# Performance work log

Hardware: AMD Instinct MI355X
Metric: run time of the kernel (lower is better)

The kernel has to match this reference:

```python
import jax, jax.numpy as jnp
import numpy as np

N, D, H, G = 4096, 256, 4, 16
HEAD_DIM = D // H
LN_EPS = 1e-5
TEMP = 5.0


def setup_inputs() -> dict:
    key = jax.random.key(0)
    ks = jax.random.split(key, 12)
    s = 0.05  # weight init scale
    nrm = lambda k, shp: jax.random.normal(k, shp, jnp.float32) * s
    return {
        "x": jax.random.normal(ks[0], (N, D), jnp.float32),
        "Wq": nrm(ks[1], (D, D)), "bq": jnp.zeros((D,), jnp.float32),
        "Wk": nrm(ks[2], (D, D)), "bk": jnp.zeros((D,), jnp.float32),
        "Wv": nrm(ks[3], (D, D)), "bv": jnp.zeros((D,), jnp.float32),
        "Wv1": nrm(ks[4], (D, D // 2)), "bv1": jnp.zeros((D // 2,), jnp.float32),
        "Wv2": nrm(ks[5], (D // 2, 1)), "bv2": jnp.zeros((1,), jnp.float32),
        "Wc1": nrm(ks[6], (2 * D, D)), "bc1": jnp.zeros((D,), jnp.float32),
        "Wc2": nrm(ks[7], (D, 1)), "bc2": jnp.zeros((1,), jnp.float32),
        "gamma": jnp.ones((D,), jnp.float32),
        "beta": jnp.zeros((D,), jnp.float32),
        "batch": jnp.sort(jax.random.randint(ks[8], (N,), 0, G)),
    }


def reference(x, Wq, bq, Wk, bk, Wv, bv, Wv1, bv1, Wv2, bv2,
              Wc1, bc1, Wc2, bc2, gamma, beta, batch):
    n = x.shape[0]
    # multi-head projections -> [N, H, head_dim]
    Q = (x @ Wq + bq).reshape(n, H, HEAD_DIM)
    K = (x @ Wk + bk).reshape(n, H, HEAD_DIM)
    V = (x @ Wv + bv).reshape(n, H, HEAD_DIM)

    # dense scores [N, N, H], block-diagonal mask by graph membership
    scores = jnp.einsum('nhd,mhd->nmh', Q, K) / np.sqrt(HEAD_DIM).astype(np.float32)
    same_graph = (batch[:, None] == batch[None, :])  # [N, N]
    scores = jnp.where(same_graph[:, :, None], scores, -jnp.inf)
    probs = jax.nn.softmax(scores, axis=1)  # softmax over keys m (dim=1, as in torch)
    # dropout is identity in eval mode
    attended = jnp.einsum('nmh,mhd->nhd', probs, V).reshape(n, D)

    # vulnerability detector MLP: D -> D/2 -> 1, sigmoid
    vuln = jax.nn.sigmoid(jax.nn.relu(x @ Wv1 + bv1) @ Wv2 + bv2)[:, 0]

    # global max pool per graph, broadcast back to nodes
    graph_ctx = jax.ops.segment_max(x, batch, num_segments=G, indices_are_sorted=True)[batch]
    combined = jnp.concatenate([x, graph_ctx], axis=1)  # [N, 2D]
    ctx = jax.nn.sigmoid(jnp.tanh(combined @ Wc1 + bc1) @ Wc2 + bc2)[:, 0]

    mha_avg = probs.mean(axis=(1, 2))  # [N]
    w = 0.6 * vuln + 0.3 * ctx + 0.1 * mha_avg

    # per-graph segment softmax with temperature 5.0
    w5 = w * TEMP
    seg_max = jax.ops.segment_max(w5, batch, num_segments=G, indices_are_sorted=True)[batch]
    e = jnp.exp(w5 - seg_max)
    seg_sum = jax.ops.segment_sum(e, batch, num_segments=G, indices_are_sorted=True)[batch]
    att = e / seg_sum  # [N]

    out = attended * att[:, None] + x  # residual
    # LayerNorm over last dim
    mu = out.mean(axis=-1, keepdims=True)
    var = out.var(axis=-1, keepdims=True)
    out = (out - mu) * jax.lax.rsqrt(var + LN_EPS) * gamma + beta
    return out, att
```

## Files before the change

kernel.cpp:

```cpp
#include <hip/hip_runtime.h>
#include <math.h>

#define N_NODES 4096
#define DIM 256
#define NH 4
#define NG 16
#define LN_EPS 1e-5f
#define TEMP 5.0f
#define RSLACK 4160
#define PS_STRIDE 72
#define BS_STRIDE 264
#define QT_MAX 24
#define K2_ATTN_BLOCKS (NG * QT_MAX)

typedef __attribute__((ext_vector_type(8))) short short8;
typedef __attribute__((ext_vector_type(4))) short short4_t;
typedef __attribute__((ext_vector_type(4))) float f32x4;

__device__ __forceinline__ unsigned short f2bf(float f) {
    unsigned u = __builtin_bit_cast(unsigned, f);
    u += 0x7FFFu + ((u >> 16) & 1u);
    return (unsigned short)(u >> 16);
}
__device__ __forceinline__ float bf2f(unsigned short u) {
    return __builtin_bit_cast(float, (unsigned)u << 16);
}
__device__ __forceinline__ float fsigmoid(float z) { return 1.f / (1.f + __expf(-z)); }
__device__ __forceinline__ float ftanh(float z) {
    float t = __expf(2.f * z);
    return (t - 1.f) / (t + 1.f);
}
__device__ __forceinline__ int seg_search(const int* __restrict__ batch, int g) {
    int lo = 0, hi = N_NODES;
    while (lo < hi) {
        int mid = (lo + hi) >> 1;
        if (batch[mid] < g) lo = mid + 1; else hi = mid;
    }
    return lo;
}

__device__ __forceinline__ short8 afrag_f32(const float* __restrict__ x, int row, int k0) {
    float4 a = *(const float4*)&x[(size_t)row * 256 + k0];
    float4 b = *(const float4*)&x[(size_t)row * 256 + k0 + 4];
    short8 r = {(short)f2bf(a.x), (short)f2bf(a.y), (short)f2bf(a.z), (short)f2bf(a.w),
                (short)f2bf(b.x), (short)f2bf(b.y), (short)f2bf(b.z), (short)f2bf(b.w)};
    return r;
}

__device__ __forceinline__ void ldsB(const float* __restrict__ W, int ws, int bn,
                                     unsigned short* __restrict__ Bs) {
    int c4 = (threadIdx.x & 15) * 4;
    int r0 = threadIdx.x >> 4;
    for (int p = 0; p < 16; ++p) {
        int k = p * 16 + r0;
        float4 wv = *(const float4*)&W[(size_t)k * ws + bn + c4];
        Bs[(c4 + 0) * BS_STRIDE + k] = f2bf(wv.x);
        Bs[(c4 + 1) * BS_STRIDE + k] = f2bf(wv.y);
        Bs[(c4 + 2) * BS_STRIDE + k] = f2bf(wv.z);
        Bs[(c4 + 3) * BS_STRIDE + k] = f2bf(wv.w);
    }
    __syncthreads();
}

__global__ __launch_bounds__(256) void k1_kernel(
    const float* __restrict__ x,
    const float* __restrict__ Wq, const float* __restrict__ bq,
    const float* __restrict__ Wk, const float* __restrict__ bk,
    const float* __restrict__ Wv, const float* __restrict__ bv,
    const float* __restrict__ Wv1, const float* __restrict__ bv1,
    const float* __restrict__ Wv2, const float* __restrict__ Wc1,
    const float* __restrict__ bc1, const int* __restrict__ batch,
    unsigned short* __restrict__ Qb, unsigned short* __restrict__ Kb,
    unsigned short* __restrict__ Vt, float* __restrict__ vacc2,
    float* __restrict__ Tpre, float* __restrict__ gcw, int* __restrict__ seg) {
    __shared__ __align__(16) char smem[64 * BS_STRIDE * 2];
    int id = blockIdx.x, tid = threadIdx.x;
    if (id < 16) {
        int g = id;
        int s = seg_search(batch, g), e = seg_search(batch, g + 1);
        float* red = (float*)smem;
        float* gl  = (float*)smem + 1024;
        int c4 = (tid & 63) * 4, way = tid >> 6;
        float4 mx = {-INFINITY, -INFINITY, -INFINITY, -INFINITY};
#pragma unroll 8
        for (int i = s + way; i < e; i += 4) {
            float4 v = *(const float4*)&x[(size_t)i * DIM + c4];
            mx.x = fmaxf(mx.x, v.x); mx.y = fmaxf(mx.y, v.y);
            mx.z = fmaxf(mx.z, v.z); mx.w = fmaxf(mx.w, v.w);
        }
        *(float4*)&red[way * 256 + c4] = mx;
        __syncthreads();
        if (way == 0) {
#pragma unroll
            for (int j = 0; j < 4; ++j) {
                float mm = fmaxf(fmaxf(red[c4 + j], red[256 + c4 + j]),
                                 fmaxf(red[512 + c4 + j], red[768 + c4 + j]));
                gl[c4 + j] = bf2f(f2bf(mm));
            }
        }
        __syncthreads();
        float ac[4] = {0.f, 0.f, 0.f, 0.f};
        for (int kb = 0; kb < 256; kb += 32) {
            float v[32];
#pragma unroll
            for (int j = 0; j < 32; ++j)
                v[j] = Wc1[(size_t)(256 + kb + j) * 256 + tid];
#pragma unroll
            for (int j = 0; j < 32; ++j) ac[j & 3] += gl[kb + j] * v[j];
        }
        gcw[g * 256 + tid] = (ac[0] + ac[1]) + (ac[2] + ac[3]);
        return;
    }
    if (id == 16) {
        if (tid <= NG) seg[tid] = seg_search(batch, tid);
        return;
    }
    int u = id - 17;
    unsigned short* Bs = (unsigned short*)smem;
    int w = tid >> 6, lane = tid & 63, m = lane & 15, quad = lane >> 4;
    if (u < 768) {
        int z = u >> 8, r = u & 255, bx = r & 63, by = r >> 6;
        const float* W = (z == 0) ? Wq : (z == 1) ? Wk : Wv;
        const float* bias = (z == 0) ? bq : (z == 1) ? bk : bv;
        ldsB(W, 256, by * 64, Bs);
        int rowA = bx * 64 + 16 * w + m;
        short8 a[8];
#pragma unroll
        for (int ks = 0; ks < 8; ++ks) a[ks] = afrag_f32(x, rowA, ks * 32 + quad * 8);
        int node0 = bx * 64 + 16 * w + quad * 4;
#pragma unroll
        for (int nt = 0; nt < 4; ++nt) {
            f32x4 acc = {0.f, 0.f, 0.f, 0.f};
#pragma unroll
            for (int ks = 0; ks < 8; ++ks) {
                short8 b = *(const short8*)&Bs[(nt * 16 + m) * BS_STRIDE + ks * 32 + quad * 8];
                acc = __builtin_amdgcn_mfma_f32_16x16x32_bf16(a[ks], b, acc, 0, 0, 0);
            }
            int col = by * 64 + nt * 16 + m;
            float bb = bias[col];
            if (z == 0) {
#pragma unroll
                for (int r2 = 0; r2 < 4; ++r2)
                    Qb[(size_t)(node0 + r2) * 256 + col] = f2bf((acc[r2] + bb) * 0.125f);
            } else if (z == 1) {
#pragma unroll
                for (int r2 = 0; r2 < 4; ++r2)
                    Kb[(size_t)(node0 + r2) * 256 + col] = f2bf(acc[r2] + bb);
            } else {
                short4_t pk = {(short)f2bf(acc[0] + bb), (short)f2bf(acc[1] + bb),
                               (short)f2bf(acc[2] + bb), (short)f2bf(acc[3] + bb)};
                *(short4_t*)&Vt[(size_t)col * RSLACK + node0] = pk;
            }
        }
    } else if (u < 896) {
        int r = u - 768, bx = r & 63, by = r >> 6;
        ldsB(Wv1, 128, by * 64, Bs);
        int rowA = bx * 64 + 16 * w + m;
        short8 a[8];
#pragma unroll
        for (int ks = 0; ks < 8; ++ks) a[ks] = afrag_f32(x, rowA, ks * 32 + quad * 8);
        int node0 = bx * 64 + 16 * w + quad * 4;
        float psum[4] = {0.f, 0.f, 0.f, 0.f};
#pragma unroll
        for (int nt = 0; nt < 4; ++nt) {
            f32x4 acc = {0.f, 0.f, 0.f, 0.f};
#pragma unroll
            for (int ks = 0; ks < 8; ++ks) {
                short8 b = *(const short8*)&Bs[(nt * 16 + m) * BS_STRIDE + ks * 32 + quad * 8];
                acc = __builtin_amdgcn_mfma_f32_16x16x32_bf16(a[ks], b, acc, 0, 0, 0);
            }
            int col = by * 64 + nt * 16 + m;
            float bb = bv1[col], wv = Wv2[col];
#pragma unroll
            for (int r2 = 0; r2 < 4; ++r2) psum[r2] += fmaxf(acc[r2] + bb, 0.f) * wv;
        }
#pragma unroll
        for (int r2 = 0; r2 < 4; ++r2) {
#pragma unroll
            for (int mm = 1; mm < 16; mm <<= 1) psum[r2] += __shfl_xor(psum[r2], mm);
            if (m == 0) vacc2[(size_t)(node0 + r2) * 2 + by] = psum[r2];
        }
    } else {
        int r = u - 896, bx = r & 63, by = r >> 6;
        ldsB(Wc1, 256, by * 64, Bs);
        int rowA = bx * 64 + 16 * w + m;
        short8 a[8];
#pragma unroll
        for (int ks = 0; ks < 8; ++ks) a[ks] = afrag_f32(x, rowA, ks * 32 + quad * 8);
        int node0 = bx * 64 + 16 * w + quad * 4;
#pragma unroll
        for (int nt = 0; nt < 4; ++nt) {
            f32x4 acc = {0.f, 0.f, 0.f, 0.f};
#pragma unroll
            for (int ks = 0; ks < 8; ++ks) {
                short8 b = *(const short8*)&Bs[(nt * 16 + m) * BS_STRIDE + ks * 32 + quad * 8];
                acc = __builtin_amdgcn_mfma_f32_16x16x32_bf16(a[ks], b, acc, 0, 0, 0);
            }
            int col = by * 64 + nt * 16 + m;
            float bb = bc1[col];
#pragma unroll
            for (int r2 = 0; r2 < 4; ++r2)
                Tpre[(size_t)(node0 + r2) * 256 + col] = acc[r2] + bb;
        }
    }
}

__global__ __launch_bounds__(256) void k2_kernel(
    const float* __restrict__ Tpre, const float* __restrict__ gcw,
    const float* __restrict__ Wc2, const int* __restrict__ batch,
    const unsigned short* __restrict__ Qb, const unsigned short* __restrict__ Kb,
    const unsigned short* __restrict__ Vt, const int* __restrict__ seg,
    unsigned short* __restrict__ Opart, float* __restrict__ Lpart,
    float* __restrict__ cacc) {
    __shared__ __align__(16) unsigned short Ps[4 * 16 * PS_STRIDE];
    int tid = threadIdx.x;
    if (blockIdx.x >= K2_ATTN_BLOCKS) {
        int id2 = blockIdx.x - K2_ATTN_BLOCKS;
        int nl = tid >> 4, cs = (tid & 15) * 16;
        int node = id2 * 16 + nl;
        int g = batch[node];
        float sum = 0.f;
#pragma unroll
        for (int j = 0; j < 16; ++j) {
            int c = cs + j;
            sum += ftanh(Tpre[(size_t)node * 256 + c] + gcw[g * 256 + c]) * Wc2[c];
        }
#pragma unroll
        for (int mm = 1; mm < 16; mm <<= 1) sum += __shfl_xor(sum, mm);
        if ((tid & 15) == 0) cacc[node] = sum;
        return;
    }
    int w = tid >> 6, lane = tid & 63, m = lane & 15, quad = lane >> 4;
    int wid = blockIdx.x * 4 + w;
    int g = wid / (QT_MAX * NH);
    int r2i = wid - g * (QT_MAX * NH);
    int qt = r2i >> 2, h = r2i & 3;
    int s = seg[g], e = seg[g + 1];
    int q0 = s + qt * 16;
    if (q0 >= e) return;

    short8 qa0 = *(const short8*)&Qb[(size_t)(q0 + m) * 256 + h * 64 + quad * 8];
    short8 qa1 = *(const short8*)&Qb[(size_t)(q0 + m) * 256 + h * 64 + 32 + quad * 8];
    short8 ones = {16256, 16256, 16256, 16256, 16256, 16256, 16256, 16256};
    f32x4 O[4];
    f32x4 Lacc = {0.f, 0.f, 0.f, 0.f};
#pragma unroll
    for (int nt = 0; nt < 4; ++nt) O[nt] = (f32x4){0.f, 0.f, 0.f, 0.f};
    int wbase = w * 16 * PS_STRIDE;

    for (int k0 = s; k0 < e; k0 += 64) {
        f32x4 S[4];
#pragma unroll
        for (int nt = 0; nt < 4; ++nt) {
            int key = k0 + nt * 16 + m;
            short8 kb0 = *(const short8*)&Kb[(size_t)key * 256 + h * 64 + quad * 8];
            short8 kb1 = *(const short8*)&Kb[(size_t)key * 256 + h * 64 + 32 + quad * 8];
            f32x4 sa = {0.f, 0.f, 0.f, 0.f};
            sa = __builtin_amdgcn_mfma_f32_16x16x32_bf16(qa0, kb0, sa, 0, 0, 0);
            sa = __builtin_amdgcn_mfma_f32_16x16x32_bf16(qa1, kb1, sa, 0, 0, 0);
            S[nt] = sa;
        }
        short8 vb[4][2];
#pragma unroll
        for (int nt = 0; nt < 4; ++nt) {
            const unsigned short* vrow = &Vt[(size_t)(h * 64 + nt * 16 + m) * RSLACK + k0];
            vb[nt][0] = *(const short8*)&vrow[quad * 8];
            vb[nt][1] = *(const short8*)&vrow[32 + quad * 8];
        }
        __builtin_amdgcn_wave_barrier();
#pragma unroll
        for (int nt = 0; nt < 4; ++nt) {
            bool valid = (k0 + nt * 16 + m) < e;
#pragma unroll
            for (int r3 = 0; r3 < 4; ++r3) {
                float p = valid ? __expf(S[nt][r3]) : 0.f;
                Ps[wbase + (quad * 4 + r3) * PS_STRIDE + nt * 16 + m] = f2bf(p);
            }
        }
        __builtin_amdgcn_wave_barrier();
        short8 pa0 = *(const short8*)&Ps[wbase + m * PS_STRIDE + quad * 8];
        short8 pa1 = *(const short8*)&Ps[wbase + m * PS_STRIDE + 32 + quad * 8];
        Lacc = __builtin_amdgcn_mfma_f32_16x16x32_bf16(pa0, ones, Lacc, 0, 0, 0);
        Lacc = __builtin_amdgcn_mfma_f32_16x16x32_bf16(pa1, ones, Lacc, 0, 0, 0);
#pragma unroll
        for (int nt = 0; nt < 4; ++nt) {
            O[nt] = __builtin_amdgcn_mfma_f32_16x16x32_bf16(pa0, vb[nt][0], O[nt], 0, 0, 0);
            O[nt] = __builtin_amdgcn_mfma_f32_16x16x32_bf16(pa1, vb[nt][1], O[nt], 0, 0, 0);
        }
    }
#pragma unroll
    for (int r3 = 0; r3 < 4; ++r3) {
        int q = q0 + quad * 4 + r3;
        if (q < e) {
            if (m == 0) Lpart[(size_t)q * 4 + h] = Lacc[r3];
#pragma unroll
            for (int nt = 0; nt < 4; ++nt)
                Opart[(size_t)q * 256 + h * 64 + nt * 16 + m] = f2bf(O[nt][r3]);
        }
    }
}

__global__ __launch_bounds__(256) void k3_kernel(
    const unsigned short* __restrict__ Opart, const float* __restrict__ Lpart,
    const float* __restrict__ x, const float* __restrict__ vacc2,
    const float* __restrict__ cacc, const float* __restrict__ bv2,
    const float* __restrict__ bc2, const float* __restrict__ gamma,
    const float* __restrict__ beta, const int* __restrict__ batch,
    const int* __restrict__ seg, float* __restrict__ out,
    float* __restrict__ att_out) {
    __shared__ float wsc[776];
    __shared__ float gm[8], gsum[8];
    __shared__ float r1[4], r2[4];
    int tid = threadIdx.x;
    int n0 = blockIdx.x * 8;
    int gf = batch[n0], gl = batch[n0 + 7];
    int s0 = seg[gf], e1 = seg[gl + 1];
    float vb = bv2[0], cb = bc2[0];
    for (int j = s0 + tid; j < e1; j += 256) {
        float2 vv = *(const float2*)&vacc2[(size_t)j * 2];
        wsc[j - s0] = TEMP * (0.6f * fsigmoid(vv.x + vv.y + vb) +
                              0.3f * fsigmoid(cacc[j] + cb) + 0.1f / 4096.f);
    }
    __syncthreads();
    for (int g = gf; g <= gl; ++g) {
        int gs_ = seg[g], ge = seg[g + 1];
        float mx = -1e30f;
        for (int j = gs_ + tid; j < ge; j += 256) mx = fmaxf(mx, wsc[j - s0]);
#pragma unroll
        for (int k2 = 32; k2; k2 >>= 1) mx = fmaxf(mx, __shfl_xor(mx, k2));
        if ((tid & 63) == 0) r1[tid >> 6] = mx;
        __syncthreads();
        mx = fmaxf(fmaxf(r1[0], r1[1]), fmaxf(r1[2], r1[3]));
        float sm = 0.f;
        for (int j = gs_ + tid; j < ge; j += 256) sm += __expf(wsc[j - s0] - mx);
#pragma unroll
        for (int k2 = 32; k2; k2 >>= 1) sm += __shfl_xor(sm, k2);
        __syncthreads();
        if ((tid & 63) == 0) r2[tid >> 6] = sm;
        __syncthreads();
        if (tid == 0) {
            gm[g - gf] = mx;
            gsum[g - gf] = r2[0] + r2[1] + r2[2] + r2[3];
        }
        __syncthreads();
    }
    int h = tid >> 6;
    for (int i = 0; i < 8; ++i) {
        int n = n0 + i;
        int g = batch[n];
        float att_n = __expf(wsc[n - s0] - gm[g - gf]) / gsum[g - gf];
        if (tid == 0) att_out[n] = att_n;
        float L = Lpart[(size_t)n * 4 + h];
        float O = bf2f(Opart[(size_t)n * 256 + tid]);
        float o = (O / L) * att_n + x[(size_t)n * 256 + tid];
        float s1 = o, s2 = o * o;
#pragma unroll
        for (int k2 = 32; k2; k2 >>= 1) {
            s1 += __shfl_xor(s1, k2);
            s2 += __shfl_xor(s2, k2);
        }
        __syncthreads();
        if ((tid & 63) == 0) { r1[tid >> 6] = s1; r2[tid >> 6] = s2; }
        __syncthreads();
        float mu = (r1[0] + r1[1] + r1[2] + r1[3]) * (1.f / 256.f);
        float ms = (r2[0] + r2[1] + r2[2] + r2[3]) * (1.f / 256.f);
        float rs = rsqrtf(ms - mu * mu + LN_EPS);
        out[(size_t)n * 256 + tid] = (o - mu) * rs * gamma[tid] + beta[tid];
    }
}

extern "C" void kernel_launch(void* const* d_in, const int* in_sizes, int n_in,
                              void* d_out, int out_size, void* d_ws, size_t ws_size,
                              hipStream_t stream) {
    const float* x     = (const float*)d_in[0];
    const float* Wq    = (const float*)d_in[1];
    const float* bq    = (const float*)d_in[2];
    const float* Wk    = (const float*)d_in[3];
    const float* bk    = (const float*)d_in[4];
    const float* Wv    = (const float*)d_in[5];
    const float* bv    = (const float*)d_in[6];
    const float* Wv1   = (const float*)d_in[7];
    const float* bv1   = (const float*)d_in[8];
    const float* Wv2   = (const float*)d_in[9];
    const float* bv2   = (const float*)d_in[10];
    const float* Wc1   = (const float*)d_in[11];
    const float* bc1   = (const float*)d_in[12];
    const float* Wc2   = (const float*)d_in[13];
    const float* bc2   = (const float*)d_in[14];
    const float* gamma = (const float*)d_in[15];
    const float* beta  = (const float*)d_in[16];
    const int*   batch = (const int*)d_in[17];

    float* out = (float*)d_out;
    float* att = out + N_NODES * DIM;

    float* vacc2 = (float*)d_ws;
    float* cacc  = vacc2 + N_NODES * 2;
    float* gcw   = cacc + N_NODES;
    float* Lpart = gcw + NG * DIM;
    float* Tpre  = Lpart + N_NODES * 4;
    int*   seg   = (int*)(Tpre + N_NODES * DIM);
    unsigned short* Qb    = (unsigned short*)(seg + 32);
    unsigned short* Kb    = Qb + RSLACK * DIM;
    unsigned short* Vt    = Kb + RSLACK * DIM;
    unsigned short* Opart = Vt + DIM * RSLACK;

    k1_kernel<<<1169, 256, 0, stream>>>(x, Wq, bq, Wk, bk, Wv, bv, Wv1, bv1, Wv2,
                                        Wc1, bc1, batch, Qb, Kb, Vt, vacc2, Tpre,
                                        gcw, seg);
    k2_kernel<<<K2_ATTN_BLOCKS + 256, 256, 0, stream>>>(Tpre, gcw, Wc2, batch,
                                                        Qb, Kb, Vt, seg,
                                                        Opart, Lpart, cacc);
    k3_kernel<<<N_NODES / 8, 256, 0, stream>>>(Opart, Lpart, x, vacc2, cacc,
                                               bv2, bc2, gamma, beta, batch, seg,
                                               out, att);
}
```

Measured before the change: 167.1 us.

## Split attention key range across blocks and reduce partial outputs in epilogue

The attention kernel now assigns each block one 64-key chunk (up to six chunks per graph) for one 16-query tile, with the four waves covering the four heads, instead of each wave looping over every key of its graph. Unnormalized partial outputs and row sums are written per chunk and summed in the LayerNorm kernel, and the block index is swizzled across the grid. This is meant to expose more parallelism and shorten the serial key loop on each wave. In exchange it writes and rereads up to six times as much bf16 partial output, launches many more blocks that exit early when a chunk falls beyond the graph, and assumes no graph has more than 384 nodes.

```diff
diff --git a/kernel.cpp b/kernel.cpp
--- a/kernel.cpp
+++ b/kernel.cpp
@@ -11,7 +11,8 @@
 #define PS_STRIDE 72
 #define BS_STRIDE 264
 #define QT_MAX 24
-#define K2_ATTN_BLOCKS (NG * QT_MAX)
+#define KC6 6
+#define K2_ATTN_BLOCKS (NG * QT_MAX * KC6)
 
 typedef __attribute__((ext_vector_type(8))) short short8;
 typedef __attribute__((ext_vector_type(4))) short short4_t;
@@ -230,72 +231,75 @@
         if ((tid & 15) == 0) cacc[node] = sum;
         return;
     }
+    int bid = (blockIdx.x & 7) * (K2_ATTN_BLOCKS / 8) + (blockIdx.x >> 3);
     int w = tid >> 6, lane = tid & 63, m = lane & 15, quad = lane >> 4;
-    int wid = blockIdx.x * 4 + w;
-    int g = wid / (QT_MAX * NH);
-    int r2i = wid - g * (QT_MAX * NH);
-    int qt = r2i >> 2, h = r2i & 3;
+    int g = bid / (QT_MAX * KC6);
+    int r1 = bid - g * (QT_MAX * KC6);
+    int kc = r1 / QT_MAX;
+    int qt = r1 - kc * QT_MAX;
+    int h = w;
     int s = seg[g], e = seg[g + 1];
     int q0 = s + qt * 16;
-    if (q0 >= e) return;
+    int kst = s + kc * 64;
+    if (q0 >= e || kst >= e) return;
 
     short8 qa0 = *(const short8*)&Qb[(size_t)(q0 + m) * 256 + h * 64 + quad * 8];
     short8 qa1 = *(const short8*)&Qb[(size_t)(q0 + m) * 256 + h * 64 + 32 + quad * 8];
+    short8 kb[4][2], vb[4][2];
+#pragma unroll
+    for (int nt = 0; nt < 4; ++nt) {
+        int key = kst + nt * 16 + m;
+        kb[nt][0] = *(const short8*)&Kb[(size_t)key * 256 + h * 64 + quad * 8];
+        kb[nt][1] = *(const short8*)&Kb[(size_t)key * 256 + h * 64 + 32 + quad * 8];
+    }
+#pragma unroll
+    for (int nt = 0; nt < 4; ++nt) {
+        const unsigned short* vrow = &Vt[(size_t)(h * 64 + nt * 16 + m) * RSLACK + kst];
+        vb[nt][0] = *(const short8*)&vrow[quad * 8];
+        vb[nt][1] = *(const short8*)&vrow[32 + quad * 8];
+    }
+
+    f32x4 S[4];
+#pragma unroll
+    for (int nt = 0; nt < 4; ++nt) {
+        f32x4 sa = {0.f, 0.f, 0.f, 0.f};
+        sa = __builtin_amdgcn_mfma_f32_16x16x32_bf16(qa0, kb[nt][0], sa, 0, 0, 0);
+        sa = __builtin_amdgcn_mfma_f32_16x16x32_bf16(qa1, kb[nt][1], sa, 0, 0, 0);
+        S[nt] = sa;
+    }
+#pragma unroll
+    for (int nt = 0; nt < 4; ++nt) {
+        bool valid = (kst + nt * 16 + m) < e;
+#pragma unroll
+        for (int r3 = 0; r3 < 4; ++r3) {
+            float p = valid ? __expf(S[nt][r3]) : 0.f;
+            Ps[w * 16 * PS_STRIDE + (quad * 4 + r3) * PS_STRIDE + nt * 16 + m] = f2bf(p);
+        }
+    }
+    __builtin_amdgcn_wave_barrier();
+    short8 pa0 = *(const short8*)&Ps[w * 16 * PS_STRIDE + m * PS_STRIDE + quad * 8];
+    short8 pa1 = *(const short8*)&Ps[w * 16 * PS_STRIDE + m * PS_STRIDE + 32 + quad * 8];
     short8 ones = {16256, 16256, 16256, 16256, 16256, 16256, 16256, 16256};
+    f32x4 Lacc = {0.f, 0.f, 0.f, 0.f};
+    Lacc = __builtin_amdgcn_mfma_f32_16x16x32_bf16(pa0, ones, Lacc, 0, 0, 0);
+    Lacc = __builtin_amdgcn_mfma_f32_16x16x32_bf16(pa1, ones, Lacc, 0, 0, 0);
     f32x4 O[4];
-    f32x4 Lacc = {0.f, 0.f, 0.f, 0.f};
-#pragma unroll
-    for (int nt = 0; nt < 4; ++nt) O[nt] = (f32x4){0.f, 0.f, 0.f, 0.f};
-    int wbase = w * 16 * PS_STRIDE;
-
-    for (int k0 = s; k0 < e; k0 += 64) {
-        f32x4 S[4];
-#pragma unroll
-        for (int nt = 0; nt < 4; ++nt) {
-            int key = k0 + nt * 16 + m;
-            short8 kb0 = *(const short8*)&Kb[(size_t)key * 256 + h * 64 + quad * 8];
-            short8 kb1 = *(const short8*)&Kb[(size_t)key * 256 + h * 64 + 32 + quad * 8];
-            f32x4 sa = {0.f, 0.f, 0.f, 0.f};
-            sa = __builtin_amdgcn_mfma_f32_16x16x32_bf16(qa0, kb0, sa, 0, 0, 0);
-            sa = __builtin_amdgcn_mfma_f32_16x16x32_bf16(qa1, kb1, sa, 0, 0, 0);
-            S[nt] = sa;
-        }
-        short8 vb[4][2];
-#pragma unroll
-        for (int nt = 0; nt < 4; ++nt) {
-            const unsigned short* vrow = &Vt[(size_t)(h * 64 + nt * 16 + m) * RSLACK + k0];
-            vb[nt][0] = *(const short8*)&vrow[quad * 8];
-            vb[nt][1] = *(const short8*)&vrow[32 + quad * 8];
-        }
-        __builtin_amdgcn_wave_barrier();
-#pragma unroll
-        for (int nt = 0; nt < 4; ++nt) {
-            bool valid = (k0 + nt * 16 + m) < e;
-#pragma unroll
-            for (int r3 = 0; r3 < 4; ++r3) {
-                float p = valid ? __expf(S[nt][r3]) : 0.f;
-                Ps[wbase + (quad * 4 + r3) * PS_STRIDE + nt * 16 + m] = f2bf(p);
-            }
-        }
-        __builtin_amdgcn_wave_barrier();
-        short8 pa0 = *(const short8*)&Ps[wbase + m * PS_STRIDE + quad * 8];
-        short8 pa1 = *(const short8*)&Ps[wbase + m * PS_STRIDE + 32 + quad * 8];
-        Lacc = __builtin_amdgcn_mfma_f32_16x16x32_bf16(pa0, ones, Lacc, 0, 0, 0);
-        Lacc = __builtin_amdgcn_mfma_f32_16x16x32_bf16(pa1, ones, Lacc, 0, 0, 0);
-#pragma unroll
-        for (int nt = 0; nt < 4; ++nt) {
-            O[nt] = __builtin_amdgcn_mfma_f32_16x16x32_bf16(pa0, vb[nt][0], O[nt], 0, 0, 0);
-            O[nt] = __builtin_amdgcn_mfma_f32_16x16x32_bf16(pa1, vb[nt][1], O[nt], 0, 0, 0);
-        }
+#pragma unroll
+    for (int nt = 0; nt < 4; ++nt) {
+        f32x4 oa = {0.f, 0.f, 0.f, 0.f};
+        oa = __builtin_amdgcn_mfma_f32_16x16x32_bf16(pa0, vb[nt][0], oa, 0, 0, 0);
+        oa = __builtin_amdgcn_mfma_f32_16x16x32_bf16(pa1, vb[nt][1], oa, 0, 0, 0);
+        O[nt] = oa;
     }
 #pragma unroll
     for (int r3 = 0; r3 < 4; ++r3) {
         int q = q0 + quad * 4 + r3;
         if (q < e) {
-            if (m == 0) Lpart[(size_t)q * 4 + h] = Lacc[r3];
+            if (m == 0) Lpart[((size_t)kc * N_NODES + q) * 4 + h] = Lacc[r3];
 #pragma unroll
             for (int nt = 0; nt < 4; ++nt)
-                Opart[(size_t)q * 256 + h * 64 + nt * 16 + m] = f2bf(O[nt][r3]);
+                Opart[((size_t)kc * N_NODES + q) * 256 + h * 64 + nt * 16 + m] =
+                    f2bf(O[nt][r3]);
         }
     }
 }
@@ -348,10 +352,17 @@
     for (int i = 0; i < 8; ++i) {
         int n = n0 + i;
         int g = batch[n];
+        int s = seg[g], e = seg[g + 1];
         float att_n = __expf(wsc[n - s0] - gm[g - gf]) / gsum[g - gf];
         if (tid == 0) att_out[n] = att_n;
-        float L = Lpart[(size_t)n * 4 + h];
-        float O = bf2f(Opart[(size_t)n * 256 + tid]);
+        float L = 0.f, O = 0.f;
+#pragma unroll
+        for (int c = 0; c < KC6; ++c) {
+            bool valid = (s + c * 64) < e;
+            float lv = Lpart[((size_t)c * N_NODES + n) * 4 + h];
+            float ov = bf2f(Opart[((size_t)c * N_NODES + n) * 256 + tid]);
+            if (valid) { L += lv; O += ov; }
+        }
         float o = (O / L) * att_n + x[(size_t)n * 256 + tid];
         float s1 = o, s2 = o * o;
 #pragma unroll
@@ -398,7 +409,7 @@
     float* cacc  = vacc2 + N_NODES * 2;
     float* gcw   = cacc + N_NODES;
     float* Lpart = gcw + NG * DIM;
-    float* Tpre  = Lpart + N_NODES * 4;
+    float* Tpre  = Lpart + KC6 * N_NODES * 4;
     int*   seg   = (int*)(Tpre + N_NODES * DIM);
     unsigned short* Qb    = (unsigned short*)(seg + 32);
     unsigned short* Kb    = Qb + RSLACK * DIM;
```

Measured after the change: 158.6 us. -5.1%, faster.

## Stage K/V tiles in LDS shared across heads and two query tiles per block

Applied to the files above, without the earlier changes.

The attention part of k2 now assigns one block per (graph, 32-query pair) with each wave handling one head. Per 64-key step the block cooperatively loads the full K tile (all heads) and the V^T tile into shared memory, and each wave reuses them for two 16-query tiles. Previously each wave read K and V straight from global memory for a single 16-query tile. The goal is to cut redundant global/L2 traffic, at the cost of block-wide barriers, extra LDS use (about 70 KB), and fewer attention blocks. Blocks are also interleaved across graphs.

```diff
diff --git a/kernel.cpp b/kernel.cpp
--- a/kernel.cpp
+++ b/kernel.cpp
@@ -10,8 +10,8 @@
 #define RSLACK 4160
 #define PS_STRIDE 72
 #define BS_STRIDE 264
-#define QT_MAX 24
-#define K2_ATTN_BLOCKS (NG * QT_MAX)
+#define QP_MAX 12
+#define K2_ATTN_BLOCKS (NG * QP_MAX)
 
 typedef __attribute__((ext_vector_type(8))) short short8;
 typedef __attribute__((ext_vector_type(4))) short short4_t;
@@ -212,6 +212,8 @@
     const unsigned short* __restrict__ Vt, const int* __restrict__ seg,
     unsigned short* __restrict__ Opart, float* __restrict__ Lpart,
     float* __restrict__ cacc) {
+    __shared__ __align__(16) unsigned short Ks[64 * BS_STRIDE];
+    __shared__ __align__(16) unsigned short Vs[256 * PS_STRIDE];
     __shared__ __align__(16) unsigned short Ps[4 * 16 * PS_STRIDE];
     int tid = threadIdx.x;
     if (blockIdx.x >= K2_ATTN_BLOCKS) {
@@ -230,72 +232,99 @@
         if ((tid & 15) == 0) cacc[node] = sum;
         return;
     }
+    int xw = blockIdx.x & 7, y = blockIdx.x >> 3;
+    int g = xw * 2 + (y >= QP_MAX);
+    int qp = (y >= QP_MAX) ? y - QP_MAX : y;
     int w = tid >> 6, lane = tid & 63, m = lane & 15, quad = lane >> 4;
-    int wid = blockIdx.x * 4 + w;
-    int g = wid / (QT_MAX * NH);
-    int r2i = wid - g * (QT_MAX * NH);
-    int qt = r2i >> 2, h = r2i & 3;
+    int h = w;
     int s = seg[g], e = seg[g + 1];
-    int q0 = s + qt * 16;
+    int q0 = s + qp * 32;
     if (q0 >= e) return;
 
-    short8 qa0 = *(const short8*)&Qb[(size_t)(q0 + m) * 256 + h * 64 + quad * 8];
-    short8 qa1 = *(const short8*)&Qb[(size_t)(q0 + m) * 256 + h * 64 + 32 + quad * 8];
+    short8 qa[2][2];
+#pragma unroll
+    for (int t = 0; t < 2; ++t) {
+        qa[t][0] = *(const short8*)&Qb[(size_t)(q0 + t * 16 + m) * 256 + h * 64 + quad * 8];
+        qa[t][1] = *(const short8*)&Qb[(size_t)(q0 + t * 16 + m) * 256 + h * 64 + 32 + quad * 8];
+    }
     short8 ones = {16256, 16256, 16256, 16256, 16256, 16256, 16256, 16256};
-    f32x4 O[4];
-    f32x4 Lacc = {0.f, 0.f, 0.f, 0.f};
-#pragma unroll
-    for (int nt = 0; nt < 4; ++nt) O[nt] = (f32x4){0.f, 0.f, 0.f, 0.f};
+    f32x4 O[2][4];
+    f32x4 Lacc[2] = {{0.f, 0.f, 0.f, 0.f}, {0.f, 0.f, 0.f, 0.f}};
+#pragma unroll
+    for (int t = 0; t < 2; ++t)
+#pragma unroll
+        for (int nt = 0; nt < 4; ++nt) O[t][nt] = (f32x4){0.f, 0.f, 0.f, 0.f};
     int wbase = w * 16 * PS_STRIDE;
-
-    for (int k0 = s; k0 < e; k0 += 64) {
-        f32x4 S[4];
-#pragma unroll
-        for (int nt = 0; nt < 4; ++nt) {
-            int key = k0 + nt * 16 + m;
-            short8 kb0 = *(const short8*)&Kb[(size_t)key * 256 + h * 64 + quad * 8];
-            short8 kb1 = *(const short8*)&Kb[(size_t)key * 256 + h * 64 + 32 + quad * 8];
-            f32x4 sa = {0.f, 0.f, 0.f, 0.f};
-            sa = __builtin_amdgcn_mfma_f32_16x16x32_bf16(qa0, kb0, sa, 0, 0, 0);
-            sa = __builtin_amdgcn_mfma_f32_16x16x32_bf16(qa1, kb1, sa, 0, 0, 0);
-            S[nt] = sa;
-        }
-        short8 vb[4][2];
-#pragma unroll
-        for (int nt = 0; nt < 4; ++nt) {
-            const unsigned short* vrow = &Vt[(size_t)(h * 64 + nt * 16 + m) * RSLACK + k0];
-            vb[nt][0] = *(const short8*)&vrow[quad * 8];
-            vb[nt][1] = *(const short8*)&vrow[32 + quad * 8];
-        }
-        __builtin_amdgcn_wave_barrier();
-#pragma unroll
-        for (int nt = 0; nt < 4; ++nt) {
-            bool valid = (k0 + nt * 16 + m) < e;
-#pragma unroll
-            for (int r3 = 0; r3 < 4; ++r3) {
-                float p = valid ? __expf(S[nt][r3]) : 0.f;
-                Ps[wbase + (quad * 4 + r3) * PS_STRIDE + nt * 16 + m] = f2bf(p);
-            }
-        }
-        __builtin_amdgcn_wave_barrier();
-        short8 pa0 = *(const short8*)&Ps[wbase + m * PS_STRIDE + quad * 8];
-        short8 pa1 = *(const short8*)&Ps[wbase + m * PS_STRIDE + 32 + quad * 8];
-        Lacc = __builtin_amdgcn_mfma_f32_16x16x32_bf16(pa0, ones, Lacc, 0, 0, 0);
-        Lacc = __builtin_amdgcn_mfma_f32_16x16x32_bf16(pa1, ones, Lacc, 0, 0, 0);
-#pragma unroll
-        for (int nt = 0; nt < 4; ++nt) {
-            O[nt] = __builtin_amdgcn_mfma_f32_16x16x32_bf16(pa0, vb[nt][0], O[nt], 0, 0, 0);
-            O[nt] = __builtin_amdgcn_mfma_f32_16x16x32_bf16(pa1, vb[nt][1], O[nt], 0, 0, 0);
-        }
-    }
-#pragma unroll
-    for (int r3 = 0; r3 < 4; ++r3) {
-        int q = q0 + quad * 4 + r3;
-        if (q < e) {
-            if (m == 0) Lpart[(size_t)q * 4 + h] = Lacc[r3];
-#pragma unroll
-            for (int nt = 0; nt < 4; ++nt)
-                Opart[(size_t)q * 256 + h * 64 + nt * 16 + m] = f2bf(O[nt][r3]);
+    int kr = tid >> 2, kc0 = (tid & 3) * 64;
+    int voff = (tid & 7) * 8, vdr = tid >> 3;
+
+    for (int kst = s; kst < e; kst += 64) {
+        {
+            const short8* ksrc = (const short8*)&Kb[(size_t)(kst + kr) * 256 + kc0];
+            unsigned short* kdst = &Ks[kr * BS_STRIDE + kc0];
+#pragma unroll
+            for (int j = 0; j < 8; ++j) {
+                int jj = (j + (tid & 3) * 2) & 7;
+                *(short8*)&kdst[jj * 8] = ksrc[jj];
+            }
+        }
+#pragma unroll
+        for (int p = 0; p < 8; ++p) {
+            int d = p * 32 + vdr;
+            *(short8*)&Vs[d * PS_STRIDE + voff] =
+                *(const short8*)&Vt[(size_t)d * RSLACK + kst + voff];
+        }
+        __syncthreads();
+#pragma unroll
+        for (int t = 0; t < 2; ++t) {
+            if (q0 + t * 16 < e) {
+                f32x4 S[4];
+#pragma unroll
+                for (int nt = 0; nt < 4; ++nt) {
+                    short8 kf0 = *(const short8*)&Ks[(nt * 16 + m) * BS_STRIDE + h * 64 + quad * 8];
+                    short8 kf1 = *(const short8*)&Ks[(nt * 16 + m) * BS_STRIDE + h * 64 + 32 + quad * 8];
+                    f32x4 sa = {0.f, 0.f, 0.f, 0.f};
+                    sa = __builtin_amdgcn_mfma_f32_16x16x32_bf16(qa[t][0], kf0, sa, 0, 0, 0);
+                    sa = __builtin_amdgcn_mfma_f32_16x16x32_bf16(qa[t][1], kf1, sa, 0, 0, 0);
+                    S[nt] = sa;
+                }
+                __builtin_amdgcn_wave_barrier();
+#pragma unroll
+                for (int nt = 0; nt < 4; ++nt) {
+                    bool valid = (kst + nt * 16 + m) < e;
+#pragma unroll
+                    for (int r3 = 0; r3 < 4; ++r3) {
+                        float p = valid ? __expf(S[nt][r3]) : 0.f;
+                        Ps[wbase + (quad * 4 + r3) * PS_STRIDE + nt * 16 + m] = f2bf(p);
+                    }
+                }
+                __builtin_amdgcn_wave_barrier();
+                short8 pa0 = *(const short8*)&Ps[wbase + m * PS_STRIDE + quad * 8];
+                short8 pa1 = *(const short8*)&Ps[wbase + m * PS_STRIDE + 32 + quad * 8];
+                Lacc[t] = __builtin_amdgcn_mfma_f32_16x16x32_bf16(pa0, ones, Lacc[t], 0, 0, 0);
+                Lacc[t] = __builtin_amdgcn_mfma_f32_16x16x32_bf16(pa1, ones, Lacc[t], 0, 0, 0);
+#pragma unroll
+                for (int nt = 0; nt < 4; ++nt) {
+                    short8 vf0 = *(const short8*)&Vs[(h * 64 + nt * 16 + m) * PS_STRIDE + quad * 8];
+                    short8 vf1 = *(const short8*)&Vs[(h * 64 + nt * 16 + m) * PS_STRIDE + 32 + quad * 8];
+                    O[t][nt] = __builtin_amdgcn_mfma_f32_16x16x32_bf16(pa0, vf0, O[t][nt], 0, 0, 0);
+                    O[t][nt] = __builtin_amdgcn_mfma_f32_16x16x32_bf16(pa1, vf1, O[t][nt], 0, 0, 0);
+                }
+            }
+        }
+        __syncthreads();
+    }
+#pragma unroll
+    for (int t = 0; t < 2; ++t) {
+#pragma unroll
+        for (int r3 = 0; r3 < 4; ++r3) {
+            int q = q0 + t * 16 + quad * 4 + r3;
+            if (q < e) {
+                if (m == 0) Lpart[(size_t)q * 4 + h] = Lacc[t][r3];
+#pragma unroll
+                for (int nt = 0; nt < 4; ++nt)
+                    Opart[(size_t)q * 256 + h * 64 + nt * 16 + m] = f2bf(O[t][nt][r3]);
+            }
         }
     }
 }
```

Result: faster. 141.1 us (-15.5%).
